# Kernel optimization log

Measured on AMD Instinct MI355X. Metric: run time of the kernel, lower is better.

Reference implementation:

```python
import jax, jax.numpy as jnp
import numpy as np

B, N, C, H = 16, 207, 64, 64

def setup_inputs() -> dict:
    key = jax.random.key(0)
    k1, k2, k3, k4, k5 = jax.random.split(key, 5)
    return {
        "x": jax.random.normal(k1, (B, N, C), dtype=jnp.float32),
        "state": jax.random.normal(k2, (B, N, 1, H), dtype=jnp.float32),
        "Wx": jax.random.normal(k3, (B, N, C, 3 * H), dtype=jnp.float32) * 0.1,
        "Wh": jax.random.normal(k4, (B, N, H, 3 * H), dtype=jnp.float32) * 0.1,
        "b": jax.random.normal(k5, (B, N, 1, 3 * H), dtype=jnp.float32) * 0.1,
    }

def reference(x, state, Wx, Wh, b):
    # x: [B,N,C] -> [B,N,1,C]; state (h): [B,N,1,H]
    if x.ndim == 3:
        x = x[..., None, :]
    h = state
    dim_hidden = Wh.shape[-2]
    # One fused batched matmul for x @ Wx, then split into r/z/c parts.
    xW = jnp.matmul(x, Wx)  # [B,N,1,3H]
    xr, xz, xc = jnp.split(xW, 3, axis=-1)
    Wrh, Wzh, Wch = jnp.split(Wh, 3, axis=-1)
    br, bz, bc = jnp.split(b, 3, axis=-1)
    r = jax.nn.sigmoid(xr + jnp.matmul(h, Wrh) + br)
    z = jax.nn.sigmoid(xz + jnp.matmul(h, Wzh) + bz)
    # Note torch precedence: r * h @ Wch == (r * h) @ Wch
    hc = jnp.tanh(xc + jnp.matmul(r * h, Wch) + bc)
    h_new = (1.0 - z) * h + z * hc  # [B,N,1,H]
    return h_new
```

## Files before the change

### kernel.cpp

```cpp
#include <hip/hip_runtime.h>
#include <math.h>


#define GC 64
#define GH 64
#define J3 192
#define WPP (GC * J3)

__global__ __launch_bounds__(192) void gru_cell_v2(
    const float* __restrict__ x,
    const float* __restrict__ state,
    const float* __restrict__ Wx,
    const float* __restrict__ Wh,
    const float* __restrict__ b,
    float* __restrict__ out)
{
    const int pos = blockIdx.x;
    const int t = threadIdx.x;
    const int jg = t % 48;
    const int rp = t / 48;

    __shared__ float x_s[GC];
    __shared__ float h_s[GH];
    __shared__ float wch_s[GC * GH];
    __shared__ float part[4][J3 + 4];
    __shared__ float rh_s[GH];
    __shared__ float z_s[GH];

    if (t < GC)           x_s[t]      = x[(size_t)pos * GC + t];
    else if (t < GC + GH) h_s[t - GC] = state[(size_t)pos * GH + (t - GC)];
    __syncthreads();

    const float4* __restrict__ Wx4 = (const float4*)(Wx + (size_t)pos * WPP);
    const float4* __restrict__ Wh4 = (const float4*)(Wh + (size_t)pos * WPP);

    float4 acc = {0.f, 0.f, 0.f, 0.f};
    const bool gate = (jg < 32);
    const int wchcol = 4 * (jg - 32);

    #pragma unroll 4
    for (int i = 0; i < 16; ++i) {
        const int c = 4 * i + rp;
        float4 wx4 = Wx4[i * J3 + t];
        float4 wh4 = Wh4[i * J3 + t];
        const float xs = x_s[c];
        acc.x += xs * wx4.x; acc.y += xs * wx4.y;
        acc.z += xs * wx4.z; acc.w += xs * wx4.w;
        if (gate) {
            const float hs = h_s[c];
            acc.x += hs * wh4.x; acc.y += hs * wh4.y;
            acc.z += hs * wh4.z; acc.w += hs * wh4.w;
        } else {
            *((float4*)&wch_s[c * GH + wchcol]) = wh4;
        }
    }

    *((float4*)&part[rp][4 * jg]) = acc;
    __syncthreads();

    float v = part[0][t] + part[1][t] + part[2][t] + part[3][t]
            + b[(size_t)pos * J3 + t];
    const float tc = v;
    if (t < GH) {
        float r = 1.f / (1.f + expf(-v));
        rh_s[t] = r * h_s[t];
    } else if (t < 2 * GH) {
        z_s[t - GH] = 1.f / (1.f + expf(-v));
    }
    __syncthreads();

    if (t >= 2 * GH) {
        const int jc = t - 2 * GH;
        float s = 0.f;
        #pragma unroll 8
        for (int k = 0; k < GH; ++k) s += rh_s[k] * wch_s[k * GH + jc];
        const float hc = tanhf(tc + s);
        const float z = z_s[jc];
        out[(size_t)pos * GH + jc] = (1.f - z) * h_s[jc] + z * hc;
    }
}

extern "C" void kernel_launch(void* const* d_in, const int* in_sizes, int n_in,
                              void* d_out, int out_size, void* d_ws, size_t ws_size,
                              hipStream_t stream) {
    const float* x     = (const float*)d_in[0];
    const float* state = (const float*)d_in[1];
    const float* Wx    = (const float*)d_in[2];
    const float* Wh    = (const float*)d_in[3];
    const float* b     = (const float*)d_in[4];
    float* out = (float*)d_out;

    const int npos = in_sizes[0] / GC;

    gru_cell_v2<<<npos, 192, 0, stream>>>(x, state, Wx, Wh, b, out);
}
```

Measured before the change: 338.2 us.

## Drop Wch shared staging; re-read candidate weights from global after gates

Removes the 16KB shared buffer for the candidate-gate Wh slice. Gate threads now compute x·Wx + h·Wh together, and candidate threads compute only x·Wx. The candidate columns of Wh are re-read straight from global memory (strided by 192 floats) after r is known. Thread mapping changes to interleave the 4 row partitions within adjacent lanes, the bias load is hoisted before the first barrier, and launch bounds request 8 blocks per CU. Lower shared memory should raise occupancy on this bandwidth-bound kernel. The cost is that the candidate Wh reads are now uncoalesced scalar loads issued late, on the critical path.

```diff
diff --git a/kernel.cpp b/kernel.cpp
--- a/kernel.cpp
+++ b/kernel.cpp
@@ -7,7 +7,7 @@
 #define J3 192
 #define WPP (GC * J3)
 
-__global__ __launch_bounds__(192) void gru_cell_v2(
+__global__ __launch_bounds__(192, 8) void gru_cell_v3(
     const float* __restrict__ x,
     const float* __restrict__ state,
     const float* __restrict__ Wx,
@@ -17,50 +17,55 @@
 {
     const int pos = blockIdx.x;
     const int t = threadIdx.x;
-    const int jg = t % 48;
-    const int rp = t / 48;
+    const int rp = t & 3;
+    const int jg = t >> 2;
 
     __shared__ float x_s[GC];
     __shared__ float h_s[GH];
-    __shared__ float wch_s[GC * GH];
     __shared__ float part[4][J3 + 4];
     __shared__ float rh_s[GH];
     __shared__ float z_s[GH];
 
     if (t < GC)           x_s[t]      = x[(size_t)pos * GC + t];
     else if (t < GC + GH) h_s[t - GC] = state[(size_t)pos * GH + (t - GC)];
+
+    const float bv = b[(size_t)pos * J3 + t];
     __syncthreads();
 
     const float4* __restrict__ Wx4 = (const float4*)(Wx + (size_t)pos * WPP);
     const float4* __restrict__ Wh4 = (const float4*)(Wh + (size_t)pos * WPP);
 
     float4 acc = {0.f, 0.f, 0.f, 0.f};
-    const bool gate = (jg < 32);
-    const int wchcol = 4 * (jg - 32);
+    const bool gate = (t < 2 * GH);
 
-    #pragma unroll 4
-    for (int i = 0; i < 16; ++i) {
-        const int c = 4 * i + rp;
-        float4 wx4 = Wx4[i * J3 + t];
-        float4 wh4 = Wh4[i * J3 + t];
-        const float xs = x_s[c];
-        acc.x += xs * wx4.x; acc.y += xs * wx4.y;
-        acc.z += xs * wx4.z; acc.w += xs * wx4.w;
-        if (gate) {
+    if (gate) {
+        #pragma unroll 4
+        for (int i = 0; i < 16; ++i) {
+            const int c = 4 * i + rp;
+            float4 wx4 = Wx4[(size_t)c * 48 + jg];
+            float4 wh4 = Wh4[(size_t)c * 48 + jg];
+            const float xs = x_s[c];
             const float hs = h_s[c];
-            acc.x += hs * wh4.x; acc.y += hs * wh4.y;
-            acc.z += hs * wh4.z; acc.w += hs * wh4.w;
-        } else {
-            *((float4*)&wch_s[c * GH + wchcol]) = wh4;
+            acc.x += xs * wx4.x + hs * wh4.x;
+            acc.y += xs * wx4.y + hs * wh4.y;
+            acc.z += xs * wx4.z + hs * wh4.z;
+            acc.w += xs * wx4.w + hs * wh4.w;
+        }
+    } else {
+        #pragma unroll 8
+        for (int i = 0; i < 16; ++i) {
+            const int c = 4 * i + rp;
+            float4 wx4 = Wx4[(size_t)c * 48 + jg];
+            const float xs = x_s[c];
+            acc.x += xs * wx4.x; acc.y += xs * wx4.y;
+            acc.z += xs * wx4.z; acc.w += xs * wx4.w;
         }
     }
 
     *((float4*)&part[rp][4 * jg]) = acc;
     __syncthreads();
 
-    float v = part[0][t] + part[1][t] + part[2][t] + part[3][t]
-            + b[(size_t)pos * J3 + t];
-    const float tc = v;
+    float v = part[0][t] + part[1][t] + part[2][t] + part[3][t] + bv;
     if (t < GH) {
         float r = 1.f / (1.f + expf(-v));
         rh_s[t] = r * h_s[t];
@@ -71,10 +76,11 @@
 
     if (t >= 2 * GH) {
         const int jc = t - 2 * GH;
+        const float* __restrict__ Wch = Wh + (size_t)pos * WPP + 2 * GH + jc;
         float s = 0.f;
         #pragma unroll 8
-        for (int k = 0; k < GH; ++k) s += rh_s[k] * wch_s[k * GH + jc];
-        const float hc = tanhf(tc + s);
+        for (int c = 0; c < GC; ++c) s += rh_s[c] * Wch[(size_t)c * J3];
+        const float hc = tanhf(v + s);
         const float z = z_s[jc];
         out[(size_t)pos * GH + jc] = (1.f - z) * h_s[jc] + z * hc;
     }
@@ -92,5 +98,5 @@
 
     const int npos = in_sizes[0] / GC;
 
-    gru_cell_v2<<<npos, 192, 0, stream>>>(x, state, Wx, Wh, b, out);
+    gru_cell_v3<<<npos, 192, 0, stream>>>(x, state, Wx, Wh, b, out);
 }
```

After: 344.4 us. No clear change (+1.8%).
